# Kernel tuning notes

Measured on AMD Instinct MI355X. Metric: run time of the kernel, lower is better.

The kernel has to match this reference:

```python
import jax, jax.numpy as jnp
import numpy as np

K = 8            # hard-attention top-k neighbors per node
NEG_SLOPE = 0.2  # leaky relu slope


def setup_inputs() -> dict:
    key = jax.random.key(0)
    k1, k2, k3, k4, k5, k6 = jax.random.split(key, 6)
    N, D, F = 50000, 64, 256
    H, O = 8, 32
    feat = jax.random.normal(k1, (N, F), dtype=jnp.float32)
    neighbors = jax.random.randint(k2, (N, D), 0, N)  # src node ids per dst
    # learned params (xavier-normal-ish scale)
    p = jax.random.normal(k3, (1, F), dtype=jnp.float32) * float(np.sqrt(2.0 / (1 + F)))
    W = jax.random.normal(k4, (F, H * O), dtype=jnp.float32) * float(np.sqrt(2.0 / (F + H * O)))
    attn_l = jax.random.normal(k5, (1, H, O), dtype=jnp.float32) * float(np.sqrt(2.0 / (H * O + 1)))
    attn_r = jax.random.normal(k6, (1, H, O), dtype=jnp.float32) * float(np.sqrt(2.0 / (H * O + 1)))
    return {"feat": feat, "neighbors": neighbors, "p": p, "W": W,
            "attn_l": attn_l, "attn_r": attn_r}


def reference(feat, neighbors, p, W, attn_l, attn_r):
    N, F = feat.shape
    H, O = attn_l.shape[1], attn_l.shape[2]
    # node projection score y = |p . x| / ||p||
    y = jnp.abs(feat @ p[0]) / jnp.linalg.norm(p)          # [N]
    # hard top-k neighbor selection by source score (select_topk on 'y')
    ys = y[neighbors]                                       # [N, D]
    _, idx = jax.lax.top_k(ys, K)                           # [N, K]
    src = jnp.take_along_axis(neighbors, idx, axis=1)       # [N, K] source ids
    # gating + projection
    gate = jax.nn.sigmoid(y) * 2.0                          # [N]
    ft = ((gate[:, None] * feat) @ W).reshape(N, H, O)      # [N, H, O]
    el = jnp.sum(ft * attn_l, axis=-1)                      # [N, H]
    er = jnp.sum(ft * attn_r, axis=-1)                      # [N, H]
    # edge scores: u_add_v, leaky_relu, edge_softmax over each dst's K edges
    e = el[src] + er[:, None, :]                            # [N, K, H]
    e = jnp.where(e > 0, e, NEG_SLOPE * e)
    a = jax.nn.softmax(e, axis=1)                           # [N, K, H]
    # u_mul_e + sum aggregation
    rst = jnp.einsum('nkh,nkho->nho', a, ft[src])           # [N, H, O]
    return jax.nn.elu(rst)
```

## Files before the change

### kernel.cpp

```cpp
#include <hip/hip_runtime.h>
#include <math.h>

#define NEG_SLOPE 0.2f

typedef _Float16 half8 __attribute__((ext_vector_type(8)));
typedef float floatx4 __attribute__((ext_vector_type(4)));

__device__ __forceinline__ float dot4f(float4 a, float4 b) {
    return a.x * b.x + a.y * b.y + a.z * b.z + a.w * b.w;
}

static __device__ __forceinline__ unsigned short f2h(float x) {
    _Float16 h = (_Float16)x;
    return __builtin_bit_cast(unsigned short, h);
}
static __device__ __forceinline__ float h2f(unsigned short u) {
    _Float16 h = __builtin_bit_cast(_Float16, u);
    return (float)h;
}

__global__ void k_prepw(const float* __restrict__ W, unsigned short* __restrict__ Wtp) {
    const int c = blockIdx.x;
    const int k = threadIdx.x;
    float v = W[(size_t)k * 256 + c];
    Wtp[(size_t)(c >> 4) * 4096 + (k >> 3) * 128 + (c & 15) * 8 + (k & 7)] = f2h(v);
}

__global__ __launch_bounds__(256) void k_fused(const float4* __restrict__ feat4,
                                               const float4* __restrict__ p4,
                                               const unsigned short* __restrict__ Wtp,
                                               const float4* __restrict__ al4,
                                               const float4* __restrict__ ar4,
                                               float* __restrict__ y,
                                               unsigned short* __restrict__ fth,
                                               float* __restrict__ el,
                                               float* __restrict__ er,
                                               int N) {
    __shared__ unsigned short As[32][264];
    const int lane = threadIdx.x & 63;
    const int w = threadIdx.x >> 6;
    const int l16 = lane & 15, quad = lane >> 4;
    const int nb = blockIdx.x * 32;

    const float4 p = p4[lane];
    float pp = dot4f(p, p);
#pragma unroll
    for (int off = 32; off; off >>= 1) pp += __shfl_xor(pp, off, 64);
    const float rnorm = 1.0f / sqrtf(pp);

#pragma unroll
    for (int j = 0; j < 8; ++j) {
        const int m = w * 8 + j;
        int n = nb + m;
        const bool valid = n < N;
        if (!valid) n = N - 1;
        float4 f = feat4[(size_t)n * 64 + lane];
        float dp = dot4f(f, p);
#pragma unroll
        for (int off = 32; off; off >>= 1) dp += __shfl_xor(dp, off, 64);
        float yv = fabsf(dp) * rnorm;
        if (lane == 0 && valid) y[n] = yv;
        float g = 2.0f / (1.0f + __expf(-yv));
        ushort4 u;
        u.x = f2h(g * f.x);
        u.y = f2h(g * f.y);
        u.z = f2h(g * f.z);
        u.w = f2h(g * f.w);
        *(ushort4*)&As[m][lane * 4] = u;
    }
    __syncthreads();

    floatx4 acc[2][4];
#pragma unroll
    for (int mt = 0; mt < 2; ++mt)
#pragma unroll
        for (int ct = 0; ct < 4; ++ct) acc[mt][ct] = (floatx4){0.f, 0.f, 0.f, 0.f};

    const unsigned short* bbase = Wtp + (size_t)(w * 4) * 4096 + quad * 128 + l16 * 8;

    for (int ks = 0; ks < 256; ks += 32) {
        half8 a0 = *(const half8*)&As[l16][ks + quad * 8];
        half8 a1 = *(const half8*)&As[16 + l16][ks + quad * 8];
        const unsigned short* bk = bbase + (ks >> 3) * 128;
        half8 b0 = *(const half8*)(bk);
        half8 b1 = *(const half8*)(bk + 4096);
        half8 b2 = *(const half8*)(bk + 8192);
        half8 b3 = *(const half8*)(bk + 12288);
        acc[0][0] = __builtin_amdgcn_mfma_f32_16x16x32_f16(a0, b0, acc[0][0], 0, 0, 0);
        acc[0][1] = __builtin_amdgcn_mfma_f32_16x16x32_f16(a0, b1, acc[0][1], 0, 0, 0);
        acc[0][2] = __builtin_amdgcn_mfma_f32_16x16x32_f16(a0, b2, acc[0][2], 0, 0, 0);
        acc[0][3] = __builtin_amdgcn_mfma_f32_16x16x32_f16(a0, b3, acc[0][3], 0, 0, 0);
        acc[1][0] = __builtin_amdgcn_mfma_f32_16x16x32_f16(a1, b0, acc[1][0], 0, 0, 0);
        acc[1][1] = __builtin_amdgcn_mfma_f32_16x16x32_f16(a1, b1, acc[1][1], 0, 0, 0);
        acc[1][2] = __builtin_amdgcn_mfma_f32_16x16x32_f16(a1, b2, acc[1][2], 0, 0, 0);
        acc[1][3] = __builtin_amdgcn_mfma_f32_16x16x32_f16(a1, b3, acc[1][3], 0, 0, 0);
    }

    __syncthreads();
#pragma unroll
    for (int mt = 0; mt < 2; ++mt)
#pragma unroll
        for (int ct = 0; ct < 4; ++ct)
#pragma unroll
            for (int i = 0; i < 4; ++i) {
                int row = mt * 16 + quad * 4 + i;
                int col = w * 64 + ct * 16 + l16;
                unsigned short h = f2h(acc[mt][ct][i]);
                As[row][col] = h;
                int grow = nb + row;
                if (grow < N) fth[(size_t)grow * 256 + col] = h;
            }
    __syncthreads();

#pragma unroll
    for (int t2 = 0; t2 < 2; ++t2) {
        const int m = threadIdx.x & 31;
        const int h = (threadIdx.x >> 5) & 7;
        const float4* att = t2 ? ar4 : al4;
        float d = 0.f;
#pragma unroll
        for (int o4 = 0; o4 < 8; ++o4) {
            ushort4 u = *(const ushort4*)&As[m][h * 32 + o4 * 4];
            float4 a = att[h * 8 + o4];
            d += h2f(u.x) * a.x + h2f(u.y) * a.y + h2f(u.z) * a.z + h2f(u.w) * a.w;
        }
        int n = nb + m;
        if (n < N) (t2 ? er : el)[(size_t)n * 8 + h] = d;
    }
}

__global__ __launch_bounds__(256) void k_aggr(const int* __restrict__ nbr,
                                              const float* __restrict__ y,
                                              const uint2* __restrict__ fth2,
                                              const float* __restrict__ el,
                                              const float* __restrict__ er,
                                              float4* __restrict__ out4,
                                              int N) {
    const int lane = threadIdx.x & 63;
    const int n = blockIdx.x * 4 + (threadIdx.x >> 6);
    if (n >= N) return;
    const int h = lane >> 3;

    const int s = nbr[(size_t)n * 64 + lane];
    const unsigned int key = __float_as_uint(y[s]);

    unsigned int t = 0u;
#pragma unroll
    for (int b = 30; b >= 0; --b) {
        unsigned int cand = t | (1u << b);
        unsigned long long m = __ballot(key >= cand);
        if (__popcll(m) >= 8) t = cand;
    }
    const unsigned long long gtmask = __ballot(key > t);
    const int ngt = __popcll(gtmask);
    const unsigned long long eqmask = __ballot(key == t);
    const unsigned long long below = (1ull << lane) - 1ull;
    const int eqrank = __popcll(eqmask & below);
    const bool in8 = (key > t) | ((key == t) & (eqrank < 8 - ngt));
    unsigned long long selmask = __ballot(in8);

    int srck[8];
#pragma unroll
    for (int k = 0; k < 8; ++k) {
        int l = __ffsll((long long)selmask) - 1;
        srck[k] = __shfl(s, l, 64);
        selmask &= selmask - 1ull;
    }

    float4 ftk[8];
#pragma unroll
    for (int k = 0; k < 8; ++k) {
        uint2 v = fth2[(size_t)srck[k] * 64 + lane];
        ftk[k].x = h2f((unsigned short)(v.x & 0xffff));
        ftk[k].y = h2f((unsigned short)(v.x >> 16));
        ftk[k].z = h2f((unsigned short)(v.y & 0xffff));
        ftk[k].w = h2f((unsigned short)(v.y >> 16));
    }
    const float erv = er[(size_t)n * 8 + h];
    float e[8];
#pragma unroll
    for (int k = 0; k < 8; ++k) {
        float ev = el[(size_t)srck[k] * 8 + h] + erv;
        e[k] = ev > 0.f ? ev : NEG_SLOPE * ev;
    }

    float m = e[0];
#pragma unroll
    for (int k = 1; k < 8; ++k) m = fmaxf(m, e[k]);
    float sum = 0.f;
#pragma unroll
    for (int k = 0; k < 8; ++k) {
        e[k] = __expf(e[k] - m);
        sum += e[k];
    }
    const float inv = 1.0f / sum;

    float4 acc = make_float4(0.f, 0.f, 0.f, 0.f);
#pragma unroll
    for (int k = 0; k < 8; ++k) {
        float a = e[k] * inv;
        acc.x += a * ftk[k].x;
        acc.y += a * ftk[k].y;
        acc.z += a * ftk[k].z;
        acc.w += a * ftk[k].w;
    }
    acc.x = acc.x > 0.f ? acc.x : __expf(acc.x) - 1.f;
    acc.y = acc.y > 0.f ? acc.y : __expf(acc.y) - 1.f;
    acc.z = acc.z > 0.f ? acc.z : __expf(acc.z) - 1.f;
    acc.w = acc.w > 0.f ? acc.w : __expf(acc.w) - 1.f;
    out4[(size_t)n * 64 + lane] = acc;
}

extern "C" void kernel_launch(void* const* d_in, const int* in_sizes, int n_in,
                              void* d_out, int out_size, void* d_ws, size_t ws_size,
                              hipStream_t stream) {
    const float* feat = (const float*)d_in[0];
    const int* nbr    = (const int*)d_in[1];
    const float* p    = (const float*)d_in[2];
    const float* W    = (const float*)d_in[3];
    const float* al   = (const float*)d_in[4];
    const float* ar   = (const float*)d_in[5];
    float* out = (float*)d_out;

    const int N = in_sizes[0] / 256;

    float* y = (float*)d_ws;
    unsigned short* Wtp = (unsigned short*)(y + N);
    float* el = (float*)(Wtp + 256 * 256);
    float* er = el + (size_t)N * 8;
    unsigned short* fth = (unsigned short*)(er + (size_t)N * 8);

    k_prepw<<<256, 256, 0, stream>>>(W, Wtp);
    k_fused<<<(N + 31) / 32, 256, 0, stream>>>((const float4*)feat, (const float4*)p,
                                               Wtp, (const float4*)al, (const float4*)ar,
                                               y, fth, el, er, N);
    k_aggr<<<(N + 3) / 4, 256, 0, stream>>>(nbr, y, (const uint2*)fth, el, er,
                                            (float4*)out, N);
}
```

Before: 177.8 us.

## Compute el/er via MFMA with packed attention matrix; fp16 aggregation and nontemporal stores

```diff
diff --git a/kernel.cpp b/kernel.cpp
--- a/kernel.cpp
+++ b/kernel.cpp
@@ -4,6 +4,7 @@
 #define NEG_SLOPE 0.2f
 
 typedef _Float16 half8 __attribute__((ext_vector_type(8)));
+typedef _Float16 half2v __attribute__((ext_vector_type(2)));
 typedef float floatx4 __attribute__((ext_vector_type(4)));
 
 __device__ __forceinline__ float dot4f(float4 a, float4 b) {
@@ -19,18 +20,32 @@
     return (float)h;
 }
 
-__global__ void k_prepw(const float* __restrict__ W, unsigned short* __restrict__ Wtp) {
-    const int c = blockIdx.x;
+__global__ void k_prepw(const float* __restrict__ W,
+                        const float* __restrict__ al,
+                        const float* __restrict__ ar,
+                        unsigned short* __restrict__ Wtp,
+                        unsigned short* __restrict__ Mp) {
     const int k = threadIdx.x;
-    float v = W[(size_t)k * 256 + c];
-    Wtp[(size_t)(c >> 4) * 4096 + (k >> 3) * 128 + (c & 15) * 8 + (k & 7)] = f2h(v);
+    if (blockIdx.x < 256) {
+        const int c = blockIdx.x;
+        float v = W[(size_t)k * 256 + c];
+        Wtp[(size_t)(c >> 4) * 4096 + (k >> 3) * 128 + (c & 15) * 8 + (k & 7)] = f2h(v);
+    } else {
+        const int t = blockIdx.x - 256;
+        float v = 0.f;
+        if (t < 8) {
+            if ((k >> 5) == t) v = al[t * 32 + (k & 31)];
+        } else {
+            if ((k >> 5) == (t - 8)) v = ar[(t - 8) * 32 + (k & 31)];
+        }
+        Mp[(k >> 3) * 128 + t * 8 + (k & 7)] = f2h(v);
+    }
 }
 
 __global__ __launch_bounds__(256) void k_fused(const float4* __restrict__ feat4,
                                                const float4* __restrict__ p4,
                                                const unsigned short* __restrict__ Wtp,
-                                               const float4* __restrict__ al4,
-                                               const float4* __restrict__ ar4,
+                                               const unsigned short* __restrict__ Mp,
                                                float* __restrict__ y,
                                                unsigned short* __restrict__ fth,
                                                float* __restrict__ el,
@@ -112,20 +127,21 @@
             }
     __syncthreads();
 
-#pragma unroll
-    for (int t2 = 0; t2 < 2; ++t2) {
-        const int m = threadIdx.x & 31;
-        const int h = (threadIdx.x >> 5) & 7;
-        const float4* att = t2 ? ar4 : al4;
-        float d = 0.f;
-#pragma unroll
-        for (int o4 = 0; o4 < 8; ++o4) {
-            ushort4 u = *(const ushort4*)&As[m][h * 32 + o4 * 4];
-            float4 a = att[h * 8 + o4];
-            d += h2f(u.x) * a.x + h2f(u.y) * a.y + h2f(u.z) * a.z + h2f(u.w) * a.w;
+    if (w < 2) {
+        floatx4 d = (floatx4){0.f, 0.f, 0.f, 0.f};
+        for (int ks = 0; ks < 256; ks += 32) {
+            half8 a = *(const half8*)&As[w * 16 + l16][ks + quad * 8];
+            half8 b = *(const half8*)(Mp + (ks >> 3) * 128 + quad * 128 + l16 * 8);
+            d = __builtin_amdgcn_mfma_f32_16x16x32_f16(a, b, d, 0, 0, 0);
         }
-        int n = nb + m;
-        if (n < N) (t2 ? er : el)[(size_t)n * 8 + h] = d;
+#pragma unroll
+        for (int i = 0; i < 4; ++i) {
+            int row = nb + w * 16 + quad * 4 + i;
+            if (row < N) {
+                if (l16 < 8) el[(size_t)row * 8 + l16] = d[i];
+                else         er[(size_t)row * 8 + (l16 - 8)] = d[i];
+            }
+        }
     }
 }
 
@@ -134,7 +150,7 @@
                                               const uint2* __restrict__ fth2,
                                               const float* __restrict__ el,
                                               const float* __restrict__ er,
-                                              float4* __restrict__ out4,
+                                              floatx4* __restrict__ out4,
                                               int N) {
     const int lane = threadIdx.x & 63;
     const int n = blockIdx.x * 4 + (threadIdx.x >> 6);
@@ -167,15 +183,10 @@
         selmask &= selmask - 1ull;
     }
 
-    float4 ftk[8];
-#pragma unroll
-    for (int k = 0; k < 8; ++k) {
-        uint2 v = fth2[(size_t)srck[k] * 64 + lane];
-        ftk[k].x = h2f((unsigned short)(v.x & 0xffff));
-        ftk[k].y = h2f((unsigned short)(v.x >> 16));
-        ftk[k].z = h2f((unsigned short)(v.y & 0xffff));
-        ftk[k].w = h2f((unsigned short)(v.y >> 16));
-    }
+    uint2 vk[8];
+#pragma unroll
+    for (int k = 0; k < 8; ++k) vk[k] = fth2[(size_t)srck[k] * 64 + lane];
+
     const float erv = er[(size_t)n * 8 + h];
     float e[8];
 #pragma unroll
@@ -195,20 +206,25 @@
     }
     const float inv = 1.0f / sum;
 
-    float4 acc = make_float4(0.f, 0.f, 0.f, 0.f);
-#pragma unroll
-    for (int k = 0; k < 8; ++k) {
-        float a = e[k] * inv;
-        acc.x += a * ftk[k].x;
-        acc.y += a * ftk[k].y;
-        acc.z += a * ftk[k].z;
-        acc.w += a * ftk[k].w;
-    }
-    acc.x = acc.x > 0.f ? acc.x : __expf(acc.x) - 1.f;
-    acc.y = acc.y > 0.f ? acc.y : __expf(acc.y) - 1.f;
-    acc.z = acc.z > 0.f ? acc.z : __expf(acc.z) - 1.f;
-    acc.w = acc.w > 0.f ? acc.w : __expf(acc.w) - 1.f;
-    out4[(size_t)n * 64 + lane] = acc;
+    half2v acc0 = (half2v){(_Float16)0, (_Float16)0};
+    half2v acc1 = acc0;
+#pragma unroll
+    for (int k = 0; k < 8; ++k) {
+        _Float16 ah = (_Float16)(e[k] * inv);
+        half2v a2 = {ah, ah};
+        acc0 += a2 * __builtin_bit_cast(half2v, vk[k].x);
+        acc1 += a2 * __builtin_bit_cast(half2v, vk[k].y);
+    }
+    floatx4 r;
+    r[0] = (float)acc0[0];
+    r[1] = (float)acc0[1];
+    r[2] = (float)acc1[0];
+    r[3] = (float)acc1[1];
+    r[0] = r[0] > 0.f ? r[0] : __expf(r[0]) - 1.f;
+    r[1] = r[1] > 0.f ? r[1] : __expf(r[1]) - 1.f;
+    r[2] = r[2] > 0.f ? r[2] : __expf(r[2]) - 1.f;
+    r[3] = r[3] > 0.f ? r[3] : __expf(r[3]) - 1.f;
+    __builtin_nontemporal_store(r, &out4[(size_t)n * 64 + lane]);
 }
 
 extern "C" void kernel_launch(void* const* d_in, const int* in_sizes, int n_in,
@@ -220,20 +236,19 @@
     const float* W    = (const float*)d_in[3];
     const float* al   = (const float*)d_in[4];
     const float* ar   = (const float*)d_in[5];
-    float* out = (float*)d_out;
 
     const int N = in_sizes[0] / 256;
 
     float* y = (float*)d_ws;
     unsigned short* Wtp = (unsigned short*)(y + N);
-    float* el = (float*)(Wtp + 256 * 256);
+    unsigned short* Mp  = Wtp + 256 * 256;
+    float* el = (float*)(Mp + 32 * 128);
     float* er = el + (size_t)N * 8;
     unsigned short* fth = (unsigned short*)(er + (size_t)N * 8);
 
-    k_prepw<<<256, 256, 0, stream>>>(W, Wtp);
+    k_prepw<<<272, 256, 0, stream>>>(W, al, ar, Wtp, Mp);
     k_fused<<<(N + 31) / 32, 256, 0, stream>>>((const float4*)feat, (const float4*)p,
-                                               Wtp, (const float4*)al, (const float4*)ar,
-                                               y, fth, el, er, N);
+                                               Wtp, Mp, y, fth, el, er, N);
     k_aggr<<<(N + 3) / 4, 256, 0, stream>>>(nbr, y, (const uint2*)fth, el, er,
-                                            (float4*)out, N);
-}
+                                            (floatx4*)d_out, N);
+}
```

New measurement: 171.7 us. -3.4%, faster.
